# Performance work log

Measured on AMD Instinct MI355X. Metric: run time of the kernel, lower is better.

Reference implementation:

```python
import jax, jax.numpy as jnp
import numpy as np

HEADS = 12
DIM_HEAD = 64
WINDOW = 16
SHIFT = 1  # fixed stand-in for random.randint(0, window-1)
SCALE = DIM_HEAD ** -0.5


def window_cls_mask(n, window, shift):
    # Shifted block-diagonal mask over the n-1 non-CLS tokens, CLS attends/attended everywhere.
    size = n - 1
    idx = jnp.arange(size)
    cur = (idx - shift) % window
    left = jnp.clip(idx - cur, 0, size)
    right = jnp.clip(idx + (window - cur), 0, size)
    i = idx[:, None]  # query position
    wmask = (i >= left[None, :]) & (i < right[None, :])  # [size, size]
    full = jnp.ones((n, n), dtype=bool)
    full = full.at[1:, 1:].set(wmask)
    return full  # [n, n] bool


def setup_inputs() -> dict:
    key = jax.random.key(0)
    k1, k2, k3 = jax.random.split(key, 3)
    b, n, dim = 2, 2049, 768
    inner = HEADS * DIM_HEAD
    return {
        "x": jax.random.normal(k1, (b, n, dim), dtype=jnp.float32),
        "w_qkv": jax.random.normal(k2, (dim, 3 * inner), dtype=jnp.float32) * 0.02,
        "w_out": jax.random.normal(k3, (inner, dim), dtype=jnp.float32) * 0.02,
        "b_out": jnp.zeros((dim,), dtype=jnp.float32),
    }


def reference(x, w_qkv, w_out, b_out):
    b, n, dim = x.shape
    h, d = HEADS, DIM_HEAD
    qkv = x @ w_qkv  # [b, n, 3*h*d]
    q, k, v = jnp.split(qkv, 3, axis=-1)
    # b n (h d) -> b h n d
    reshape = lambda t: t.reshape(b, n, h, d).transpose(0, 2, 1, 3)
    q, k, v = reshape(q), reshape(k), reshape(v)
    dots = jnp.einsum('bhid,bhjd->bhij', q, k) * SCALE  # [b, h, n, n]
    mask = window_cls_mask(n, WINDOW, SHIFT)  # [n, n]
    neg = -jnp.finfo(dots.dtype).max
    dots = jnp.where(mask[None, None], dots, neg)
    attn = jax.nn.softmax(dots, axis=-1)
    out = jnp.einsum('bhij,bhjd->bhid', attn, v)  # [b, h, n, d]
    out = out.transpose(0, 2, 1, 3).reshape(b, n, h * d)
    return out @ w_out + b_out
```

## Files before the change

### kernel.cpp

```cpp
#include <hip/hip_runtime.h>
#include <hip/hip_bf16.h>
#include <math.h>

typedef __attribute__((ext_vector_type(8))) __bf16 bf16x8;
typedef __attribute__((ext_vector_type(4))) float f32x4;

#define HEADS 12
#define DHEAD 64
#define NTOK 2049
#define BATCH 2
#define DIM 768
#define QKV3 2304
#define MROWS 4098
#define MP 4224
#define ATT_SCALE 0.125f
#define BKS 64
#define NSPLIT 33
#define PSTRIDE 68

__global__ __launch_bounds__(256) void cvt_x_kernel(const float* __restrict__ x,
                                                    __bf16* __restrict__ xb) {
  int t = blockIdx.x * 256 + threadIdx.x;
  long e = (long)t * 8;
  int row = (int)(e / DIM);
  bf16x8 v;
  if (row < MROWS) {
    const float4 a = *(const float4*)(x + e);
    const float4 b = *(const float4*)(x + e + 4);
    v[0] = (__bf16)a.x; v[1] = (__bf16)a.y; v[2] = (__bf16)a.z; v[3] = (__bf16)a.w;
    v[4] = (__bf16)b.x; v[5] = (__bf16)b.y; v[6] = (__bf16)b.z; v[7] = (__bf16)b.w;
  } else {
#pragma unroll
    for (int j = 0; j < 8; ++j) v[j] = (__bf16)0.f;
  }
  *(bf16x8*)(xb + e) = v;
}

__global__ __launch_bounds__(256) void transpose_cvt_kernel(const float* __restrict__ in,
                                                            __bf16* __restrict__ out,
                                                            int R, int C) {
  __shared__ float tile[32][33];
  int c0 = blockIdx.x * 32, r0 = blockIdx.y * 32;
  int tx = threadIdx.x & 31, ty = threadIdx.x >> 5;
#pragma unroll
  for (int i = 0; i < 4; ++i) {
    int r = ty + i * 8;
    tile[r][tx] = in[(size_t)(r0 + r) * C + c0 + tx];
  }
  __syncthreads();
#pragma unroll
  for (int i = 0; i < 4; ++i) {
    int r = ty + i * 8;
    out[(size_t)(c0 + r) * R + r0 + tx] = (__bf16)tile[tx][r];
  }
}

template <bool BF16_OUT>
__global__ __launch_bounds__(256) void gemm128_kernel(const __bf16* __restrict__ A,
                                                      const __bf16* __restrict__ Bt,
                                                      void* __restrict__ Cv,
                                                      const float* __restrict__ bias,
                                                      int N, int K, int Mvalid) {
  __shared__ __bf16 sA[2][128 * BKS];
  __shared__ __bf16 sB[2][128 * BKS];
  const int tid = threadIdx.x;
  const int w = tid >> 6, lane = tid & 63;
  const int m0 = blockIdx.y * 128, n0 = blockIdx.x * 128;
  const int wr = w >> 1, wc = w & 1;
  f32x4 acc[4][4] = {};

  const int srow = (w << 5) + (lane >> 3);
  const int scol = (lane & 7) << 3;
  const __bf16* gA = A + (size_t)(m0 + srow) * K + scol;
  const __bf16* gB = Bt + (size_t)(n0 + srow) * K + scol;
  const int ldsoff0 = (w << 2) << 9;

  const int nk = K / BKS;

#define STAGE(buf, kt)                                                                   \
  do {                                                                                   \
    _Pragma("unroll")                                                                    \
    for (int it = 0; it < 4; ++it) {                                                     \
      __builtin_amdgcn_global_load_lds(                                                  \
          (const __attribute__((address_space(1))) void*)(gA + (size_t)(it * 8) * K + (kt)), \
          (__attribute__((address_space(3))) void*)(&sA[buf][ldsoff0 + (it << 9)]), 16, 0, 0); \
      __builtin_amdgcn_global_load_lds(                                                  \
          (const __attribute__((address_space(1))) void*)(gB + (size_t)(it * 8) * K + (kt)), \
          (__attribute__((address_space(3))) void*)(&sB[buf][ldsoff0 + (it << 9)]), 16, 0, 0); \
    }                                                                                    \
  } while (0)

  STAGE(0, 0);
  __syncthreads();

  for (int t = 0; t < nk; ++t) {
    const int cur = t & 1;
    if (t + 1 < nk) STAGE(cur ^ 1, (t + 1) * BKS);
    const __bf16* bufA = sA[cur];
    const __bf16* bufB = sB[cur];
#pragma unroll
    for (int kk = 0; kk < BKS; kk += 32) {
      bf16x8 af[4], bfr[4];
#pragma unroll
      for (int m = 0; m < 4; ++m)
        af[m] = *(const bf16x8*)&bufA[(wr * 64 + m * 16 + (lane & 15)) * BKS + kk + (lane >> 4) * 8];
#pragma unroll
      for (int n = 0; n < 4; ++n)
        bfr[n] = *(const bf16x8*)&bufB[(wc * 64 + n * 16 + (lane & 15)) * BKS + kk + (lane >> 4) * 8];
#pragma unroll
      for (int m = 0; m < 4; ++m)
#pragma unroll
        for (int n = 0; n < 4; ++n)
          acc[m][n] = __builtin_amdgcn_mfma_f32_16x16x32_bf16(af[m], bfr[n], acc[m][n], 0, 0, 0);
    }
    __syncthreads();
  }
#undef STAGE

#pragma unroll
  for (int m = 0; m < 4; ++m) {
#pragma unroll
    for (int n = 0; n < 4; ++n) {
      int col = n0 + wc * 64 + n * 16 + (lane & 15);
      int rbase = m0 + wr * 64 + m * 16 + ((lane >> 4) << 2);
#pragma unroll
      for (int r = 0; r < 4; ++r) {
        int row = rbase + r;
        float val = acc[m][n][r];
        if constexpr (BF16_OUT) {
          ((__bf16*)Cv)[(size_t)row * N + col] = (__bf16)val;
        } else {
          if (row < Mvalid) ((float*)Cv)[(size_t)row * N + col] = val + bias[col];
        }
      }
    }
  }
}

__global__ __launch_bounds__(64) void attn_win_kernel(const __bf16* __restrict__ qkv,
                                                      __bf16* __restrict__ attnb) {
  int bidx = blockIdx.x;
  int hg = bidx % 3; bidx /= 3;
  int blk = bidx % 129;
  int bb = bidx / 129;
  int lane = threadIdx.x;
  int h = hg * 4 + (lane >> 4);
  int qi = lane & 15;
  int t0 = (blk == 0) ? 1 : 2 + 16 * (blk - 1);
  int nt = (blk == 0) ? 1 : ((NTOK - t0) < 16 ? (NTOK - t0) : 16);
  bool active = qi < nt;
  int qt = t0 + (active ? qi : nt - 1);
  const size_t base = (size_t)bb * NTOK * QKV3;

  float q[64];
  {
    const __bf16* qp = qkv + base + (size_t)qt * QKV3 + h * DHEAD;
#pragma unroll
    for (int d0 = 0; d0 < 64; d0 += 8) {
      bf16x8 v = *(const bf16x8*)(qp + d0);
#pragma unroll
      for (int j = 0; j < 8; ++j) q[d0 + j] = (float)v[j];
    }
  }

  float s[17];
  float mx = -3.4e38f;
#pragma unroll
  for (int j = 0; j < 17; ++j) {
    int jc = (j - 1) < (nt - 1) ? (j - 1) : (nt - 1);
    int kt = (j == 0) ? 0 : t0 + jc;
    const __bf16* kp = qkv + base + (size_t)kt * QKV3 + DIM + h * DHEAD;
    float dot = 0.f;
#pragma unroll
    for (int d0 = 0; d0 < 64; d0 += 8) {
      bf16x8 v = *(const bf16x8*)(kp + d0);
#pragma unroll
      for (int jj = 0; jj < 8; ++jj) dot = fmaf(q[d0 + jj], (float)v[jj], dot);
    }
    s[j] = (j <= nt) ? dot * ATT_SCALE : -3.4e38f;
    mx = fmaxf(mx, s[j]);
  }
  float sum = 0.f;
#pragma unroll
  for (int j = 0; j < 17; ++j) {
    s[j] = expf(s[j] - mx);
    sum += s[j];
  }
  float inv = 1.f / sum;

  float o[64];
#pragma unroll
  for (int d = 0; d < 64; ++d) o[d] = 0.f;
#pragma unroll
  for (int j = 0; j < 17; ++j) {
    int jc = (j - 1) < (nt - 1) ? (j - 1) : (nt - 1);
    int vt = (j == 0) ? 0 : t0 + jc;
    const __bf16* vp = qkv + base + (size_t)vt * QKV3 + 2 * DIM + h * DHEAD;
    float p = s[j];
#pragma unroll
    for (int d0 = 0; d0 < 64; d0 += 8) {
      bf16x8 v = *(const bf16x8*)(vp + d0);
#pragma unroll
      for (int jj = 0; jj < 8; ++jj) o[d0 + jj] = fmaf(p, (float)v[jj], o[d0 + jj]);
    }
  }

  if (active) {
    __bf16* op = attnb + (size_t)(bb * NTOK + qt) * DIM + h * DHEAD;
#pragma unroll
    for (int d0 = 0; d0 < 64; d0 += 8) {
      bf16x8 v;
#pragma unroll
      for (int j = 0; j < 8; ++j) v[j] = (__bf16)(o[d0 + j] * inv);
      *(bf16x8*)(op + d0) = v;
    }
  }
}

__global__ __launch_bounds__(64) void attn_cls_part(const __bf16* __restrict__ qkv,
                                                    float* __restrict__ part) {
  int bid = blockIdx.x;
  const int sp = bid % NSPLIT;
  const int bh = bid / NSPLIT;
  const int h = bh % HEADS;
  const int bb = bh / HEADS;
  const int lane = threadIdx.x;
  const size_t base = (size_t)bb * NTOK * QKV3;

  float q[64];
  {
    const __bf16* qp = qkv + base + h * DHEAD;
#pragma unroll
    for (int d0 = 0; d0 < 64; d0 += 8) {
      bf16x8 v = *(const bf16x8*)(qp + d0);
#pragma unroll
      for (int j = 0; j < 8; ++j) q[d0 + j] = (float)v[j];
    }
  }

  const int t = sp * 64 + lane;
  const bool valid = t < NTOK;
  const int tc = valid ? t : NTOK - 1;
  float dot = 0.f;
  {
    const __bf16* kp = qkv + base + (size_t)tc * QKV3 + DIM + h * DHEAD;
#pragma unroll
    for (int d0 = 0; d0 < 64; d0 += 8) {
      bf16x8 v = *(const bf16x8*)(kp + d0);
#pragma unroll
      for (int j = 0; j < 8; ++j) dot = fmaf(q[d0 + j], (float)v[j], dot);
    }
  }
  float s = valid ? dot * ATT_SCALE : -3.4e38f;

  float m = s;
#pragma unroll
  for (int off = 32; off > 0; off >>= 1) m = fmaxf(m, __shfl_xor(m, off, 64));
  float p = valid ? expf(s - m) : 0.f;
  float l = p;
#pragma unroll
  for (int off = 32; off > 0; off >>= 1) l += __shfl_xor(l, off, 64);

  __shared__ float sp_lds[64];
  sp_lds[lane] = p;
  __syncthreads();

  const int nt = (NTOK - sp * 64) < 64 ? (NTOK - sp * 64) : 64;
  float o = 0.f;
  const __bf16* vcol = qkv + base + (size_t)(sp * 64) * QKV3 + 2 * DIM + h * DHEAD + lane;
  for (int tt = 0; tt < nt; ++tt) {
    o = fmaf(sp_lds[tt], (float)vcol[(size_t)tt * QKV3], o);
  }

  float* pb = part + ((size_t)bh * NSPLIT + sp) * PSTRIDE;
  pb[lane] = o;
  if (lane == 0) { pb[64] = m; pb[65] = l; }
}

__global__ __launch_bounds__(64) void attn_cls_reduce(const float* __restrict__ part,
                                                      __bf16* __restrict__ attnb) {
  const int bh = blockIdx.x;
  const int h = bh % HEADS;
  const int bb = bh / HEADS;
  const int lane = threadIdx.x;
  const float* pb0 = part + (size_t)bh * NSPLIT * PSTRIDE;
  float M = -3.4e38f;
#pragma unroll
  for (int i = 0; i < NSPLIT; ++i) M = fmaxf(M, pb0[i * PSTRIDE + 64]);
  float L = 0.f, o = 0.f;
#pragma unroll
  for (int i = 0; i < NSPLIT; ++i) {
    float w = expf(pb0[i * PSTRIDE + 64] - M);
    L = fmaf(pb0[i * PSTRIDE + 65], w, L);
    o = fmaf(pb0[i * PSTRIDE + lane], w, o);
  }
  attnb[(size_t)(bb * NTOK) * DIM + h * DHEAD + lane] = (__bf16)(o / L);
}

extern "C" void kernel_launch(void* const* d_in, const int* in_sizes, int n_in,
                              void* d_out, int out_size, void* d_ws, size_t ws_size,
                              hipStream_t stream) {
  const float* x = (const float*)d_in[0];
  const float* w_qkv = (const float*)d_in[1];
  const float* w_out = (const float*)d_in[2];
  const float* b_out = (const float*)d_in[3];
  float* out = (float*)d_out;

  char* ws = (char*)d_ws;
  __bf16* xb    = (__bf16*)(ws);
  __bf16* wqkvT = (__bf16*)(ws + 6488064);
  __bf16* woutT = (__bf16*)(ws + 6488064 + 3538944);
  __bf16* qkvb  = (__bf16*)(ws + 6488064 + 3538944 + 1179648);
  __bf16* attnb = (__bf16*)(ws + 6488064 + 3538944 + 1179648 + 19464192);
  float*  clsp  = (float*)(ws + 6488064 + 3538944 + 1179648 + 19464192 + 6488064);

  cvt_x_kernel<<<1584, 256, 0, stream>>>(x, xb);
  transpose_cvt_kernel<<<dim3(QKV3 / 32, DIM / 32), 256, 0, stream>>>(w_qkv, wqkvT, DIM, QKV3);
  transpose_cvt_kernel<<<dim3(DIM / 32, DIM / 32), 256, 0, stream>>>(w_out, woutT, DIM, DIM);

  gemm128_kernel<true><<<dim3(QKV3 / 128, MP / 128), 256, 0, stream>>>(
      xb, wqkvT, (void*)qkvb, nullptr, QKV3, DIM, MP);

  attn_win_kernel<<<BATCH * 129 * 3, 64, 0, stream>>>(qkvb, attnb);
  attn_cls_part<<<BATCH * HEADS * NSPLIT, 64, 0, stream>>>(qkvb, clsp);
  attn_cls_reduce<<<BATCH * HEADS, 64, 0, stream>>>(clsp, attnb);

  gemm128_kernel<false><<<dim3(DIM / 128, MP / 128), 256, 0, stream>>>(
      attnb, woutT, (void*)out, b_out, DIM, DIM, MROWS);
}
```

Baseline: 174.2 us.

## Merge prep and attention launches and XOR-swizzle GEMM LDS tiles

The x conversion and both weight transpose kernels become one prep kernel, and the window and CLS-partial attention kernels become one launch, cutting kernel launch count and inter-kernel gaps. Separately, the GEMM now XOR-swizzles the 16-byte column chunks per row when staging to LDS and reading fragments, to avoid LDS bank conflicts on the MFMA operand loads. The merged kernels branch on block index, so register and LDS use follow the heavier branch, which can reduce occupancy for the lighter one.

```diff
diff --git a/kernel.cpp b/kernel.cpp
--- a/kernel.cpp
+++ b/kernel.cpp
@@ -18,30 +18,53 @@
 #define NSPLIT 33
 #define PSTRIDE 68
 
-__global__ __launch_bounds__(256) void cvt_x_kernel(const float* __restrict__ x,
-                                                    __bf16* __restrict__ xb) {
-  int t = blockIdx.x * 256 + threadIdx.x;
-  long e = (long)t * 8;
-  int row = (int)(e / DIM);
-  bf16x8 v;
-  if (row < MROWS) {
-    const float4 a = *(const float4*)(x + e);
-    const float4 b = *(const float4*)(x + e + 4);
-    v[0] = (__bf16)a.x; v[1] = (__bf16)a.y; v[2] = (__bf16)a.z; v[3] = (__bf16)a.w;
-    v[4] = (__bf16)b.x; v[5] = (__bf16)b.y; v[6] = (__bf16)b.z; v[7] = (__bf16)b.w;
+#define CVT_BLOCKS 1584
+#define TQKV_BX 72
+#define TQKV_BLOCKS (72 * 24)
+#define TOUT_BX 24
+#define TOUT_BLOCKS (24 * 24)
+#define PREP_BLOCKS (CVT_BLOCKS + TQKV_BLOCKS + TOUT_BLOCKS)
+#define WIN_BLOCKS (BATCH * 129 * 3)
+
+__global__ __launch_bounds__(256) void prep_kernel(const float* __restrict__ x,
+                                                   const float* __restrict__ w_qkv,
+                                                   const float* __restrict__ w_out,
+                                                   __bf16* __restrict__ xb,
+                                                   __bf16* __restrict__ wqkvT,
+                                                   __bf16* __restrict__ woutT) {
+  __shared__ float tile[32][33];
+  const int b = blockIdx.x, tid = threadIdx.x;
+  if (b < CVT_BLOCKS) {
+    long e = ((long)b * 256 + tid) * 8;
+    int row = (int)(e / DIM);
+    bf16x8 v;
+    if (row < MROWS) {
+      const float4 a = *(const float4*)(x + e);
+      const float4 c = *(const float4*)(x + e + 4);
+      v[0] = (__bf16)a.x; v[1] = (__bf16)a.y; v[2] = (__bf16)a.z; v[3] = (__bf16)a.w;
+      v[4] = (__bf16)c.x; v[5] = (__bf16)c.y; v[6] = (__bf16)c.z; v[7] = (__bf16)c.w;
+    } else {
+#pragma unroll
+      for (int j = 0; j < 8; ++j) v[j] = (__bf16)0.f;
+    }
+    *(bf16x8*)(xb + e) = v;
+    return;
+  }
+  const float* in;
+  __bf16* outp;
+  int C, bx, by;
+  if (b < CVT_BLOCKS + TQKV_BLOCKS) {
+    int idx = b - CVT_BLOCKS;
+    bx = idx % TQKV_BX; by = idx / TQKV_BX;
+    in = w_qkv; outp = wqkvT; C = QKV3;
   } else {
-#pragma unroll
-    for (int j = 0; j < 8; ++j) v[j] = (__bf16)0.f;
-  }
-  *(bf16x8*)(xb + e) = v;
-}
-
-__global__ __launch_bounds__(256) void transpose_cvt_kernel(const float* __restrict__ in,
-                                                            __bf16* __restrict__ out,
-                                                            int R, int C) {
-  __shared__ float tile[32][33];
-  int c0 = blockIdx.x * 32, r0 = blockIdx.y * 32;
-  int tx = threadIdx.x & 31, ty = threadIdx.x >> 5;
+    int idx = b - CVT_BLOCKS - TQKV_BLOCKS;
+    bx = idx % TOUT_BX; by = idx / TOUT_BX;
+    in = w_out; outp = woutT; C = DIM;
+  }
+  const int R = DIM;
+  const int c0 = bx * 32, r0 = by * 32;
+  const int tx = tid & 31, ty = tid >> 5;
 #pragma unroll
   for (int i = 0; i < 4; ++i) {
     int r = ty + i * 8;
@@ -51,7 +74,7 @@
 #pragma unroll
   for (int i = 0; i < 4; ++i) {
     int r = ty + i * 8;
-    out[(size_t)(c0 + r) * R + r0 + tx] = (__bf16)tile[tx][r];
+    outp[(size_t)(c0 + r) * R + r0 + tx] = (__bf16)tile[tx][r];
   }
 }
 
@@ -70,7 +93,7 @@
   f32x4 acc[4][4] = {};
 
   const int srow = (w << 5) + (lane >> 3);
-  const int scol = (lane & 7) << 3;
+  const int scol = ((lane & 7) ^ (lane >> 3)) << 3;
   const __bf16* gA = A + (size_t)(m0 + srow) * K + scol;
   const __bf16* gB = Bt + (size_t)(n0 + srow) * K + scol;
   const int ldsoff0 = (w << 2) << 9;
@@ -93,6 +116,11 @@
   STAGE(0, 0);
   __syncthreads();
 
+  const int sw0 = ((lane >> 4) ^ (lane & 7)) << 3;
+  const int sw1 = sw0 ^ 32;
+  const int rofA = (wr * 64 + (lane & 15)) * BKS;
+  const int rofB = (wc * 64 + (lane & 15)) * BKS;
+
   for (int t = 0; t < nk; ++t) {
     const int cur = t & 1;
     if (t + 1 < nk) STAGE(cur ^ 1, (t + 1) * BKS);
@@ -100,13 +128,14 @@
     const __bf16* bufB = sB[cur];
 #pragma unroll
     for (int kk = 0; kk < BKS; kk += 32) {
+      const int so = (kk == 0) ? sw0 : sw1;
       bf16x8 af[4], bfr[4];
 #pragma unroll
       for (int m = 0; m < 4; ++m)
-        af[m] = *(const bf16x8*)&bufA[(wr * 64 + m * 16 + (lane & 15)) * BKS + kk + (lane >> 4) * 8];
+        af[m] = *(const bf16x8*)&bufA[rofA + m * 16 * BKS + so];
 #pragma unroll
       for (int n = 0; n < 4; ++n)
-        bfr[n] = *(const bf16x8*)&bufB[(wc * 64 + n * 16 + (lane & 15)) * BKS + kk + (lane >> 4) * 8];
+        bfr[n] = *(const bf16x8*)&bufB[rofB + n * 16 * BKS + so];
 #pragma unroll
       for (int m = 0; m < 4; ++m)
 #pragma unroll
@@ -137,94 +166,96 @@
   }
 }
 
-__global__ __launch_bounds__(64) void attn_win_kernel(const __bf16* __restrict__ qkv,
-                                                      __bf16* __restrict__ attnb) {
-  int bidx = blockIdx.x;
-  int hg = bidx % 3; bidx /= 3;
-  int blk = bidx % 129;
-  int bb = bidx / 129;
-  int lane = threadIdx.x;
-  int h = hg * 4 + (lane >> 4);
-  int qi = lane & 15;
-  int t0 = (blk == 0) ? 1 : 2 + 16 * (blk - 1);
-  int nt = (blk == 0) ? 1 : ((NTOK - t0) < 16 ? (NTOK - t0) : 16);
-  bool active = qi < nt;
-  int qt = t0 + (active ? qi : nt - 1);
-  const size_t base = (size_t)bb * NTOK * QKV3;
-
-  float q[64];
-  {
-    const __bf16* qp = qkv + base + (size_t)qt * QKV3 + h * DHEAD;
-#pragma unroll
-    for (int d0 = 0; d0 < 64; d0 += 8) {
-      bf16x8 v = *(const bf16x8*)(qp + d0);
-#pragma unroll
-      for (int j = 0; j < 8; ++j) q[d0 + j] = (float)v[j];
-    }
-  }
-
-  float s[17];
-  float mx = -3.4e38f;
-#pragma unroll
-  for (int j = 0; j < 17; ++j) {
-    int jc = (j - 1) < (nt - 1) ? (j - 1) : (nt - 1);
-    int kt = (j == 0) ? 0 : t0 + jc;
-    const __bf16* kp = qkv + base + (size_t)kt * QKV3 + DIM + h * DHEAD;
-    float dot = 0.f;
-#pragma unroll
-    for (int d0 = 0; d0 < 64; d0 += 8) {
-      bf16x8 v = *(const bf16x8*)(kp + d0);
-#pragma unroll
-      for (int jj = 0; jj < 8; ++jj) dot = fmaf(q[d0 + jj], (float)v[jj], dot);
-    }
-    s[j] = (j <= nt) ? dot * ATT_SCALE : -3.4e38f;
-    mx = fmaxf(mx, s[j]);
-  }
-  float sum = 0.f;
-#pragma unroll
-  for (int j = 0; j < 17; ++j) {
-    s[j] = expf(s[j] - mx);
-    sum += s[j];
-  }
-  float inv = 1.f / sum;
-
-  float o[64];
-#pragma unroll
-  for (int d = 0; d < 64; ++d) o[d] = 0.f;
-#pragma unroll
-  for (int j = 0; j < 17; ++j) {
-    int jc = (j - 1) < (nt - 1) ? (j - 1) : (nt - 1);
-    int vt = (j == 0) ? 0 : t0 + jc;
-    const __bf16* vp = qkv + base + (size_t)vt * QKV3 + 2 * DIM + h * DHEAD;
-    float p = s[j];
-#pragma unroll
-    for (int d0 = 0; d0 < 64; d0 += 8) {
-      bf16x8 v = *(const bf16x8*)(vp + d0);
-#pragma unroll
-      for (int jj = 0; jj < 8; ++jj) o[d0 + jj] = fmaf(p, (float)v[jj], o[d0 + jj]);
-    }
-  }
-
-  if (active) {
-    __bf16* op = attnb + (size_t)(bb * NTOK + qt) * DIM + h * DHEAD;
-#pragma unroll
-    for (int d0 = 0; d0 < 64; d0 += 8) {
-      bf16x8 v;
-#pragma unroll
-      for (int j = 0; j < 8; ++j) v[j] = (__bf16)(o[d0 + j] * inv);
-      *(bf16x8*)(op + d0) = v;
-    }
-  }
-}
-
-__global__ __launch_bounds__(64) void attn_cls_part(const __bf16* __restrict__ qkv,
-                                                    float* __restrict__ part) {
-  int bid = blockIdx.x;
+__global__ __launch_bounds__(64) void attn_fused_kernel(const __bf16* __restrict__ qkv,
+                                                        __bf16* __restrict__ attnb,
+                                                        float* __restrict__ part) {
+  __shared__ float sp_lds[64];
+  const int lane = threadIdx.x;
+
+  if (blockIdx.x < WIN_BLOCKS) {
+    int bidx = blockIdx.x;
+    int hg = bidx % 3; bidx /= 3;
+    int blk = bidx % 129;
+    int bb = bidx / 129;
+    int h = hg * 4 + (lane >> 4);
+    int qi = lane & 15;
+    int t0 = (blk == 0) ? 1 : 2 + 16 * (blk - 1);
+    int nt = (blk == 0) ? 1 : ((NTOK - t0) < 16 ? (NTOK - t0) : 16);
+    bool active = qi < nt;
+    int qt = t0 + (active ? qi : nt - 1);
+    const size_t base = (size_t)bb * NTOK * QKV3;
+
+    float q[64];
+    {
+      const __bf16* qp = qkv + base + (size_t)qt * QKV3 + h * DHEAD;
+#pragma unroll
+      for (int d0 = 0; d0 < 64; d0 += 8) {
+        bf16x8 v = *(const bf16x8*)(qp + d0);
+#pragma unroll
+        for (int j = 0; j < 8; ++j) q[d0 + j] = (float)v[j];
+      }
+    }
+
+    float s[17];
+    float mx = -3.4e38f;
+#pragma unroll
+    for (int j = 0; j < 17; ++j) {
+      int jc = (j - 1) < (nt - 1) ? (j - 1) : (nt - 1);
+      int kt = (j == 0) ? 0 : t0 + jc;
+      const __bf16* kp = qkv + base + (size_t)kt * QKV3 + DIM + h * DHEAD;
+      float dot = 0.f;
+#pragma unroll
+      for (int d0 = 0; d0 < 64; d0 += 8) {
+        bf16x8 v = *(const bf16x8*)(kp + d0);
+#pragma unroll
+        for (int jj = 0; jj < 8; ++jj) dot = fmaf(q[d0 + jj], (float)v[jj], dot);
+      }
+      s[j] = (j <= nt) ? dot * ATT_SCALE : -3.4e38f;
+      mx = fmaxf(mx, s[j]);
+    }
+    float sum = 0.f;
+#pragma unroll
+    for (int j = 0; j < 17; ++j) {
+      s[j] = expf(s[j] - mx);
+      sum += s[j];
+    }
+    float inv = 1.f / sum;
+
+    float o[64];
+#pragma unroll
+    for (int d = 0; d < 64; ++d) o[d] = 0.f;
+#pragma unroll
+    for (int j = 0; j < 17; ++j) {
+      int jc = (j - 1) < (nt - 1) ? (j - 1) : (nt - 1);
+      int vt = (j == 0) ? 0 : t0 + jc;
+      const __bf16* vp = qkv + base + (size_t)vt * QKV3 + 2 * DIM + h * DHEAD;
+      float p = s[j];
+#pragma unroll
+      for (int d0 = 0; d0 < 64; d0 += 8) {
+        bf16x8 v = *(const bf16x8*)(vp + d0);
+#pragma unroll
+        for (int jj = 0; jj < 8; ++jj) o[d0 + jj] = fmaf(p, (float)v[jj], o[d0 + jj]);
+      }
+    }
+
+    if (active) {
+      __bf16* op = attnb + (size_t)(bb * NTOK + qt) * DIM + h * DHEAD;
+#pragma unroll
+      for (int d0 = 0; d0 < 64; d0 += 8) {
+        bf16x8 v;
+#pragma unroll
+        for (int j = 0; j < 8; ++j) v[j] = (__bf16)(o[d0 + j] * inv);
+        *(bf16x8*)(op + d0) = v;
+      }
+    }
+    return;
+  }
+
+  int bid = blockIdx.x - WIN_BLOCKS;
   const int sp = bid % NSPLIT;
   const int bh = bid / NSPLIT;
   const int h = bh % HEADS;
   const int bb = bh / HEADS;
-  const int lane = threadIdx.x;
   const size_t base = (size_t)bb * NTOK * QKV3;
 
   float q[64];
@@ -261,7 +292,6 @@
 #pragma unroll
   for (int off = 32; off > 0; off >>= 1) l += __shfl_xor(l, off, 64);
 
-  __shared__ float sp_lds[64];
   sp_lds[lane] = p;
   __syncthreads();
 
@@ -314,15 +344,12 @@
   __bf16* attnb = (__bf16*)(ws + 6488064 + 3538944 + 1179648 + 19464192);
   float*  clsp  = (float*)(ws + 6488064 + 3538944 + 1179648 + 19464192 + 6488064);
 
-  cvt_x_kernel<<<1584, 256, 0, stream>>>(x, xb);
-  transpose_cvt_kernel<<<dim3(QKV3 / 32, DIM / 32), 256, 0, stream>>>(w_qkv, wqkvT, DIM, QKV3);
-  transpose_cvt_kernel<<<dim3(DIM / 32, DIM / 32), 256, 0, stream>>>(w_out, woutT, DIM, DIM);
+  prep_kernel<<<PREP_BLOCKS, 256, 0, stream>>>(x, w_qkv, w_out, xb, wqkvT, woutT);
 
   gemm128_kernel<true><<<dim3(QKV3 / 128, MP / 128), 256, 0, stream>>>(
       xb, wqkvT, (void*)qkvb, nullptr, QKV3, DIM, MP);
 
-  attn_win_kernel<<<BATCH * 129 * 3, 64, 0, stream>>>(qkvb, attnb);
-  attn_cls_part<<<BATCH * HEADS * NSPLIT, 64, 0, stream>>>(qkvb, clsp);
+  attn_fused_kernel<<<WIN_BLOCKS + BATCH * HEADS * NSPLIT, 64, 0, stream>>>(qkvb, attnb, clsp);
   attn_cls_reduce<<<BATCH * HEADS, 64, 0, stream>>>(clsp, attnb);
 
   gemm128_kernel<false><<<dim3(DIM / 128, MP / 128), 256, 0, stream>>>(
```

After: 156.6 us. 1.11x faster.
